# Kernel tuning notes

Hardware: AMD Instinct MI355X
Metric: run time of the kernel (lower is better)

Reference implementation:

```python
import jax, jax.numpy as jnp
import numpy as np
from jax import lax

B, D, N = 1024, 1024, 65536
M, Ks, DS = 8, 256, 128      # key PQ: subvectors, codewords, subvec dim (D/M)
MV, DV = 8, 256              # value PQ: subvectors, subvec dim (OUT/MV)
OUT = MV * DV
K_TOP = 64


def setup_inputs() -> dict:
    key = jax.random.key(0)
    ks = jax.random.split(key, 7)
    x = jax.random.normal(ks[0], (B, D), dtype=jnp.float32)
    # whitening matrix starts as identity in the module; perturb slightly for a non-trivial test
    whitening_matrix = jnp.eye(D, dtype=jnp.float32) + 0.01 * jax.random.normal(ks[1], (D, D), dtype=jnp.float32)
    key_codebooks = jax.random.normal(ks[2], (M, Ks, DS), dtype=jnp.float32)
    value_codebooks = jax.random.normal(ks[3], (MV, Ks, DV), dtype=jnp.float32)
    bias = jnp.zeros((OUT,), dtype=jnp.float32)
    key_codes = jax.random.randint(ks[4], (N, M), 0, Ks, dtype=jnp.int32)
    value_codes = jax.random.randint(ks[5], (N, MV), 0, Ks, dtype=jnp.int32)
    return {
        "x": x,
        "whitening_matrix": whitening_matrix,
        "key_codebooks": key_codebooks,
        "value_codebooks": value_codebooks,
        "bias": bias,
        "key_codes": key_codes,
        "value_codes": value_codes,
        "k": K_TOP,
    }


def reference(x, whitening_matrix, key_codebooks, value_codebooks, bias, key_codes, value_codes, k):
    # 1) whiten the query (module buffer 'whitening_matrix')
    q = x @ whitening_matrix                      # [B, D]
    qs = q.reshape(B, M, DS)                      # [B, M, DS] query subvectors

    # 2) ADC distance tables: squared L2 between each query subvector and each codeword
    #    dt[b, m, c] = ||qs[b,m] - cb[m,c]||^2
    q_sq = jnp.sum(qs * qs, axis=-1)              # [B, M]
    c_sq = jnp.sum(key_codebooks * key_codebooks, axis=-1)  # [M, Ks]
    cross = jnp.einsum("bmd,mcd->bmc", qs, key_codebooks)   # [B, M, Ks]
    dt = q_sq[:, :, None] + c_sq[None, :, :] - 2.0 * cross  # [B, M, Ks]

    # 3) asymmetric distance to all N stored keys via code gather (irregular access)
    lut = dt.transpose(1, 0, 2)                   # [M, B, Ks]
    # per-subvector gather then sum: d[b, n] = sum_m lut[m, b, key_codes[n, m]]
    dists = jax.vmap(lambda l, c: l[:, c])(lut, key_codes.T).sum(axis=0)  # [B, N]

    # 4) top-k nearest neighbors
    neg_top, top_idx = lax.top_k(-dists, k)       # [B, k]

    # 5) reconstruct values of retrieved neighbors from value PQ codebooks
    vc = value_codes[top_idx]                     # [B, k, MV] int codes
    vals = value_codebooks[jnp.arange(MV)[None, None, :], vc]  # [B, k, MV, DV]
    vals = vals.reshape(vals.shape[0], vals.shape[1], OUT)      # [B, k, OUT]

    # 6) distance-weighted aggregation (softmax over negative distances) + bias
    w = jax.nn.softmax(neg_top, axis=-1)          # [B, k]
    y = jnp.einsum("bk,bko->bo", w, vals) + bias  # [B, OUT]
    return y
```

## Files before the change

### kernel.cpp

```cpp
#include <hip/hip_runtime.h>

#define N_ITEMS 65536

__launch_bounds__(256)
__global__ void gemm_q_kernel(const float* __restrict__ A,
                              const float* __restrict__ W,
                              float* __restrict__ qpart) {
  __shared__ float As[16][132];
  __shared__ float Bs[16][132];
  const int tid = threadIdx.x;
  const int tx = tid & 15, ty = tid >> 4;
  const int rb = blockIdx.y * 128, cb = blockIdx.x * 128;
  const int kz = blockIdx.z * 256;
  const int ar = tid >> 2, ac = (tid & 3) << 2;
  const int bk = tid >> 5, bc = (tid & 31) << 2;

  float4 va0 = *(const float4*)&A[(rb + ar) * 1024 + kz + ac];
  float4 va1 = *(const float4*)&A[(rb + ar + 64) * 1024 + kz + ac];
  float4 vb0 = *(const float4*)&W[(kz + bk) * 1024 + cb + bc];
  float4 vb1 = *(const float4*)&W[(kz + bk + 8) * 1024 + cb + bc];

  float acc[8][8] = {};
  for (int k0 = 0; k0 < 256; k0 += 16) {
    As[ac + 0][ar] = va0.x; As[ac + 1][ar] = va0.y;
    As[ac + 2][ar] = va0.z; As[ac + 3][ar] = va0.w;
    As[ac + 0][ar + 64] = va1.x; As[ac + 1][ar + 64] = va1.y;
    As[ac + 2][ar + 64] = va1.z; As[ac + 3][ar + 64] = va1.w;
    *(float4*)&Bs[bk][bc] = vb0;
    *(float4*)&Bs[bk + 8][bc] = vb1;
    __syncthreads();
    if (k0 + 16 < 256) {
      va0 = *(const float4*)&A[(rb + ar) * 1024 + kz + k0 + 16 + ac];
      va1 = *(const float4*)&A[(rb + ar + 64) * 1024 + kz + k0 + 16 + ac];
      vb0 = *(const float4*)&W[(kz + k0 + 16 + bk) * 1024 + cb + bc];
      vb1 = *(const float4*)&W[(kz + k0 + 16 + bk + 8) * 1024 + cb + bc];
    }
#pragma unroll
    for (int kk = 0; kk < 16; kk++) {
      const float4 a0 = *(const float4*)&As[kk][ty << 2];
      const float4 a1 = *(const float4*)&As[kk][64 + (ty << 2)];
      const float4 b0 = *(const float4*)&Bs[kk][tx << 2];
      const float4 b1 = *(const float4*)&Bs[kk][64 + (tx << 2)];
      const float ar8[8] = {a0.x, a0.y, a0.z, a0.w, a1.x, a1.y, a1.z, a1.w};
      const float br8[8] = {b0.x, b0.y, b0.z, b0.w, b1.x, b1.y, b1.z, b1.w};
#pragma unroll
      for (int r = 0; r < 8; r++)
#pragma unroll
        for (int c = 0; c < 8; c++)
          acc[r][c] = fmaf(ar8[r], br8[c], acc[r][c]);
    }
    __syncthreads();
  }
  float* outp = qpart + blockIdx.z * 1048576;
#pragma unroll
  for (int rh = 0; rh < 2; rh++)
#pragma unroll
    for (int r = 0; r < 4; r++) {
      const int row = rb + rh * 64 + (ty << 2) + r;
      const int ri = rh * 4 + r;
      *(float4*)&outp[row * 1024 + cb + (tx << 2)] =
          make_float4(acc[ri][0], acc[ri][1], acc[ri][2], acc[ri][3]);
      *(float4*)&outp[row * 1024 + cb + 64 + (tx << 2)] =
          make_float4(acc[ri][4], acc[ri][5], acc[ri][6], acc[ri][7]);
    }
}

__launch_bounds__(256)
__global__ void lut_kernel(const float* __restrict__ qpart,
                           const float* __restrict__ kcb,
                           const int* __restrict__ key_codes,
                           float* __restrict__ lut,
                           unsigned long long* __restrict__ pcodes,
                           uint4* __restrict__ poffs) {
  if (blockIdx.z == 8) {
    const int g0 = (((int)blockIdx.y * 4 + (int)blockIdx.x) * 256 + (int)threadIdx.x) * 4;
#pragma unroll
    for (int t = 0; t < 4; t++) {
      const int gid = g0 + t;
      unsigned long long p = 0ull;
      unsigned h[8];
#pragma unroll
      for (int j = 0; j < 8; j++) {
        const unsigned c = (unsigned)key_codes[gid * 8 + j] & 255u;
        p |= (unsigned long long)c << (8 * j);
        h[j] = ((c >> 1) << 7) | ((c & 1u) << 2);
      }
      pcodes[gid] = p;
      poffs[gid] = make_uint4(h[0] | (h[1] << 16), h[2] | (h[3] << 16),
                              h[4] | (h[5] << 16), h[6] | (h[7] << 16));
    }
    return;
  }

  __shared__ float As[32][68];
  __shared__ float Bs[32][68];
  const int tid = threadIdx.x;
  const int tx = tid & 15, ty = tid >> 4;
  const int m = blockIdx.z;
  const int rb = blockIdx.y * 64;
  const int cb0 = blockIdx.x * 64;
  float acc[4][4] = {};
  float qa[4] = {}, cs[4] = {};
  for (int k0 = 0; k0 < 128; k0 += 32) {
#pragma unroll
    for (int l = 0; l < 2; l++) {
      const int e = tid + l * 256;
      const int row = e >> 3, c4 = (e & 7) << 2;
      const int qidx = (rb + row) * 1024 + m * 128 + k0 + c4;
      const float4 p0 = *(const float4*)&qpart[qidx];
      const float4 p1 = *(const float4*)&qpart[qidx + 1048576];
      const float4 p2 = *(const float4*)&qpart[qidx + 2097152];
      const float4 p3 = *(const float4*)&qpart[qidx + 3145728];
      const float4 va = make_float4(p0.x + p1.x + p2.x + p3.x,
                                    p0.y + p1.y + p2.y + p3.y,
                                    p0.z + p1.z + p2.z + p3.z,
                                    p0.w + p1.w + p2.w + p3.w);
      As[c4 + 0][row] = va.x; As[c4 + 1][row] = va.y;
      As[c4 + 2][row] = va.z; As[c4 + 3][row] = va.w;
      const float4 vb = *(const float4*)&kcb[(m * 256 + cb0 + row) * 128 + k0 + c4];
      Bs[c4 + 0][row] = vb.x; Bs[c4 + 1][row] = vb.y;
      Bs[c4 + 2][row] = vb.z; Bs[c4 + 3][row] = vb.w;
    }
    __syncthreads();
#pragma unroll
    for (int kk = 0; kk < 32; kk++) {
      const float4 a = *(const float4*)&As[kk][ty << 2];
      const float4 b = *(const float4*)&Bs[kk][tx << 2];
      const float ar[4] = {a.x, a.y, a.z, a.w};
      const float br[4] = {b.x, b.y, b.z, b.w};
#pragma unroll
      for (int r = 0; r < 4; r++)
#pragma unroll
        for (int c = 0; c < 4; c++)
          acc[r][c] = fmaf(ar[r], br[c], acc[r][c]);
#pragma unroll
      for (int r = 0; r < 4; r++) qa[r] = fmaf(ar[r], ar[r], qa[r]);
#pragma unroll
      for (int c = 0; c < 4; c++) cs[c] = fmaf(br[c], br[c], cs[c]);
    }
    __syncthreads();
  }
#pragma unroll
  for (int r = 0; r < 4; r++) {
    const int row = rb + (ty << 2) + r;
    const int col = cb0 + (tx << 2);
    float4 v;
    v.x = qa[r] + cs[0] - 2.0f * acc[r][0];
    v.y = qa[r] + cs[1] - 2.0f * acc[r][1];
    v.z = qa[r] + cs[2] - 2.0f * acc[r][2];
    v.w = qa[r] + cs[3] - 2.0f * acc[r][3];
    *(float4*)&lut[row * 2048 + m * 256 + col] = v;
  }
}

extern __shared__ char dyn_lds[];

__launch_bounds__(1024)
__global__ void scan2r_kernel(const float* __restrict__ lut,
                              const uint4* __restrict__ poffs,
                              unsigned* __restrict__ cand_d,
                              unsigned short* __restrict__ cand_n) {
  char* repb = dyn_lds;
  unsigned* repw = (unsigned*)dyn_lds;
  short* temps = (short*)(dyn_lds + 131072);
  unsigned* tempw = (unsigned*)(dyn_lds + 131072);
  const int tid = threadIdx.x;
  const int g = blockIdx.x;

  {
    const int w = tid >> 6, lane = tid & 63;
    const int rr = w & 1, seg = w >> 1;
    const int row = (g << 1) + rr;
    const int e0 = seg * 256 + lane * 4;
    const float4 v4 = *(const float4*)&lut[row * 2048 + e0];
    float s4 = v4.x + v4.y + v4.z + v4.w;
#pragma unroll
    for (int off = 32; off > 0; off >>= 1) s4 += __shfl_xor(s4, off);
    const float mean = s4 * (1.0f / 256.0f);
    const float vals[4] = {v4.x, v4.y, v4.z, v4.w};
#pragma unroll
    for (int k = 0; k < 4; k++) {
      float f = (vals[k] - mean) * 64.0f;
      f = fmaxf(fminf(f, 32000.0f), -32000.0f);
      temps[(e0 + k) * 2 + rr] = (short)(int)rintf(f);
    }
  }
  __syncthreads();

  {
    const int lane = tid & 63;
    const unsigned v0 = tempw[tid * 2];
    const unsigned v1 = tempw[tid * 2 + 1];
    const int Dbase = tid * 32;
#pragma unroll
    for (int k = 0; k < 16; k++) {
      const int r = (k + lane) & 15;
      repw[Dbase + 2 * r] = v0;
      repw[Dbase + 1 + 2 * r] = v1;
    }
  }
  __syncthreads();

  const int r = tid & 15;
  const char* base0 = repb + (r << 3);
  const char* base1 = repb + 65536 + (r << 3);
  int d0a = 0x7FFFFFFF, d1a = 0x7FFFFFFF, i0a = 0, i1a = 0;
  int d0b = 0x7FFFFFFF, d1b = 0x7FFFFFFF, i0b = 0, i1b = 0;

  uint4 oc = poffs[tid];
  uint4 nc = poffs[tid + 1024];
  for (int it = 0; it < 64; it++) {
    const int n = tid + (it << 10);
    uint4 nn2 = nc;
    if (it < 62) nn2 = poffs[n + 2048];
    unsigned wv;
    int s0, s1;
    wv = *(const unsigned*)(base0 + (oc.x & 0xFFFFu));
    s0 = (int)(short)wv; s1 = ((int)wv) >> 16;
#define LK(B, HV, OFS) { wv = *(const unsigned*)((B) + (HV) + (OFS)); \
    s0 += (int)(short)wv; s1 += ((int)wv) >> 16; }
    LK(base0, oc.x >> 16, 16384)
    LK(base0, oc.y & 0xFFFFu, 32768)
    LK(base0, oc.y >> 16, 49152)
    LK(base1, oc.z & 0xFFFFu, 0)
    LK(base1, oc.z >> 16, 16384)
    LK(base1, oc.w & 0xFFFFu, 32768)
    LK(base1, oc.w >> 16, 49152)
#undef LK
    if (s0 < d1a) {
      if (s0 < d0a) { d1a = d0a; i1a = i0a; d0a = s0; i0a = n; }
      else          { d1a = s0; i1a = n; }
    }
    if (s1 < d1b) {
      if (s1 < d0b) { d1b = d0b; i1b = i0b; d0b = s1; i0b = n; }
      else          { d1b = s1; i1b = n; }
    }
    oc = nc; nc = nn2;
  }

  {
    const int ba = (g << 1) * 2048 + tid * 2;
    *(uint2*)&cand_d[ba] = make_uint2((unsigned)(d0a + 0x40000000),
                                      (unsigned)(d1a + 0x40000000));
    *(unsigned*)&cand_n[ba] = (unsigned)i0a | ((unsigned)i1a << 16);
    const int bb = ((g << 1) + 1) * 2048 + tid * 2;
    *(uint2*)&cand_d[bb] = make_uint2((unsigned)(d0b + 0x40000000),
                                      (unsigned)(d1b + 0x40000000));
    *(unsigned*)&cand_n[bb] = (unsigned)i0b | ((unsigned)i1b << 16);
  }
}

__launch_bounds__(512)
__global__ void scan16_kernel(const float* __restrict__ lut,
                              const unsigned long long* __restrict__ pcodes,
                              unsigned* __restrict__ cand_d,
                              unsigned short* __restrict__ cand_n) {
  __shared__ short sRep[32768];
  const int tid = threadIdx.x;
  const int b = blockIdx.x;

  const float4 v4 = *(const float4*)&lut[b * 2048 + tid * 4];
  float s4 = v4.x + v4.y + v4.z + v4.w;
#pragma unroll
  for (int off = 32; off > 0; off >>= 1) s4 += __shfl_xor(s4, off);
  const float mean = s4 * (1.0f / 256.0f);

  const float vals[4] = {v4.x, v4.y, v4.z, v4.w};
#pragma unroll
  for (int k2 = 0; k2 < 4; k2++) {
    float f = (vals[k2] - mean) * 64.0f;
    f = fmaxf(fminf(f, 32000.0f), -32000.0f);
    const int iv = (int)rintf(f);
    const unsigned hw = (unsigned)(unsigned short)iv;
    const unsigned wrd = hw | (hw << 16);
    const uint4 wv = make_uint4(wrd, wrd, wrd, wrd);
    const int e = tid * 4 + k2;
    *(uint4*)&((unsigned*)sRep)[e * 8] = wv;
    *(uint4*)&((unsigned*)sRep)[e * 8 + 4] = wv;
  }
  __syncthreads();

  const int r = tid & 15;
  int d0 = 0x7FFFFFFF, d1 = 0x7FFFFFFF, d2 = 0x7FFFFFFF, d3 = 0x7FFFFFFF;
  int i0 = 0, i1 = 0, i2 = 0, i3 = 0;

  unsigned long long c8 = pcodes[tid];
  for (int it = 0; it < 128; it++) {
    const int n = tid + (it << 9);
    unsigned long long nxt = 0ull;
    if (it < 127) nxt = pcodes[n + 512];
    const unsigned lo = (unsigned)c8;
    const unsigned hi = (unsigned)(c8 >> 32);
    int s;
    s  = sRep[(((lo      ) & 255u) << 4) + r        ];
    s += sRep[(((lo >>  8) & 255u) << 4) + r +  4096];
    s += sRep[(((lo >> 16) & 255u) << 4) + r +  8192];
    s += sRep[(((lo >> 24)       ) << 4) + r + 12288];
    s += sRep[(((hi      ) & 255u) << 4) + r + 16384];
    s += sRep[(((hi >>  8) & 255u) << 4) + r + 20480];
    s += sRep[(((hi >> 16) & 255u) << 4) + r + 24576];
    s += sRep[(((hi >> 24)       ) << 4) + r + 28672];
    if (s < d3) {
      if (s < d1) {
        if (s < d0) { d3 = d2; i3 = i2; d2 = d1; i2 = i1; d1 = d0; i1 = i0; d0 = s; i0 = n; }
        else        { d3 = d2; i3 = i2; d2 = d1; i2 = i1; d1 = s; i1 = n; }
      } else {
        if (s < d2) { d3 = d2; i3 = i2; d2 = s; i2 = n; }
        else        { d3 = s; i3 = n; }
      }
    }
    c8 = nxt;
  }

  const int base = b * 2048 + tid * 4;
  const uint4 dv = make_uint4((unsigned)(d0 + 0x40000000), (unsigned)(d1 + 0x40000000),
                              (unsigned)(d2 + 0x40000000), (unsigned)(d3 + 0x40000000));
  *(uint4*)&cand_d[base] = dv;
  const unsigned ni01 = (unsigned)i0 | ((unsigned)i1 << 16);
  const unsigned ni23 = (unsigned)i2 | ((unsigned)i3 << 16);
  *(uint2*)&cand_n[base] = make_uint2(ni01, ni23);
}

__launch_bounds__(256)
__global__ void select_kernel(const unsigned* __restrict__ cand_d,
                              const unsigned short* __restrict__ cand_n,
                              const int* __restrict__ value_codes,
                              const float* __restrict__ vcb,
                              const float* __restrict__ bias,
                              float* __restrict__ out) {
  __shared__ unsigned sredw[4];
  __shared__ unsigned long long clist[256];
  __shared__ float sw[256];
  __shared__ int svc[2048];
  __shared__ int scnt;
  __shared__ float sWsum;

  const int tid = threadIdx.x;
  const int b = blockIdx.x;

  const uint4 a0 = *(const uint4*)&cand_d[b * 2048 + tid * 8];
  const uint4 a1 = *(const uint4*)&cand_d[b * 2048 + tid * 8 + 4];
  const uint4 nn = *(const uint4*)&cand_n[b * 2048 + tid * 8];
  unsigned dk[8] = {a0.x, a0.y, a0.z, a0.w, a1.x, a1.y, a1.z, a1.w};
  unsigned ni[8] = {nn.x & 0xFFFFu, nn.x >> 16, nn.y & 0xFFFFu, nn.y >> 16,
                    nn.z & 0xFFFFu, nn.z >> 16, nn.w & 0xFFFFu, nn.w >> 16};

  if (tid == 0) scnt = 0;
  unsigned mn = dk[0];
#pragma unroll
  for (int j = 1; j < 8; j++) mn = (dk[j] < mn) ? dk[j] : mn;
#pragma unroll
  for (int off = 32; off > 0; off >>= 1) {
    const unsigned o = __shfl_xor(mn, off);
    mn = (o < mn) ? o : mn;
  }
  if ((tid & 63) == 0) sredw[tid >> 6] = mn;
  __syncthreads();
  unsigned sMin = sredw[0];
  sMin = (sredw[1] < sMin) ? sredw[1] : sMin;
  sMin = (sredw[2] < sMin) ? sredw[2] : sMin;
  sMin = (sredw[3] < sMin) ? sredw[3] : sMin;
  const unsigned lim = sMin + 2048u;

  const int lane = tid & 63;
  const unsigned long long lm = (1ull << lane) - 1ull;
#pragma unroll
  for (int j = 0; j < 8; j++) {
    const bool pred = dk[j] <= lim;
    const unsigned long long mask = __ballot(pred);
    int base = 0;
    if (lane == 0 && mask) base = atomicAdd(&scnt, __popcll(mask));
    base = __shfl(base, 0);
    if (pred) {
      const int pos = base + __popcll(mask & lm);
      if (pos < 256) clist[pos] = ((unsigned long long)dk[j] << 32) | ni[j];
    }
  }
  __syncthreads();
  const int cnt = min(scnt, 256);

  if (tid < cnt) {
    const int gap = (int)((unsigned)(clist[tid] >> 32)) - (int)sMin;
    sw[tid] = __expf((float)gap * -0.015625f);
  }
  for (int i = tid; i < (cnt << 3); i += 256)
    svc[i] = value_codes[((int)(clist[i >> 3] & 0xFFFFFFFFu)) * 8 + (i & 7)];
  __syncthreads();

  if (tid < 64) {
    float s = 0.f;
    for (int j = tid; j < cnt; j += 64) s += sw[j];
#pragma unroll
    for (int off = 32; off > 0; off >>= 1) s += __shfl_xor(s, off);
    if (tid == 0) sWsum = s;
  }
  __syncthreads();
  const float inv = 1.0f / sWsum;

  const int c0 = tid << 3;
  const int mv = c0 >> 8;
  const int off = c0 & 255;
  float4 acc0 = make_float4(0.f, 0.f, 0.f, 0.f);
  float4 acc1 = make_float4(0.f, 0.f, 0.f, 0.f);
  const float* vbase = vcb + mv * 65536 + off;
  for (int k = 0; k < cnt; k++) {
    const float w = sw[k];
    const float* vp = vbase + svc[(k << 3) + mv] * 256;
    const float4 v0 = *(const float4*)vp;
    const float4 v1 = *(const float4*)(vp + 4);
    acc0.x = fmaf(w, v0.x, acc0.x); acc0.y = fmaf(w, v0.y, acc0.y);
    acc0.z = fmaf(w, v0.z, acc0.z); acc0.w = fmaf(w, v0.w, acc0.w);
    acc1.x = fmaf(w, v1.x, acc1.x); acc1.y = fmaf(w, v1.y, acc1.y);
    acc1.z = fmaf(w, v1.z, acc1.z); acc1.w = fmaf(w, v1.w, acc1.w);
  }
  const float4 b0 = *(const float4*)&bias[c0];
  const float4 b1 = *(const float4*)&bias[c0 + 4];
  *(float4*)&out[b * 2048 + c0] =
      make_float4(fmaf(acc0.x, inv, b0.x), fmaf(acc0.y, inv, b0.y),
                  fmaf(acc0.z, inv, b0.z), fmaf(acc0.w, inv, b0.w));
  *(float4*)&out[b * 2048 + c0 + 4] =
      make_float4(fmaf(acc1.x, inv, b1.x), fmaf(acc1.y, inv, b1.y),
                  fmaf(acc1.z, inv, b1.z), fmaf(acc1.w, inv, b1.w));
}

extern "C" void kernel_launch(void* const* d_in, const int* in_sizes, int n_in,
                              void* d_out, int out_size, void* d_ws, size_t ws_size,
                              hipStream_t stream) {
  const float* x    = (const float*)d_in[0];
  const float* W    = (const float*)d_in[1];
  const float* kcb  = (const float*)d_in[2];
  const float* vcb  = (const float*)d_in[3];
  const float* bias = (const float*)d_in[4];
  const int* key_codes   = (const int*)d_in[5];
  const int* value_codes = (const int*)d_in[6];
  float* out = (float*)d_out;

  float* qpart = (float*)d_ws;
  float* lut   = qpart + 4194304;
  uint4* poffs = (uint4*)(lut + 2097152);
  unsigned long long* pcodes = (unsigned long long*)(poffs + 65536);
  unsigned* cand_d = (unsigned*)d_ws;
  unsigned short* cand_n = (unsigned short*)(cand_d + 2097152);

  hipLaunchKernelGGL(gemm_q_kernel, dim3(8, 8, 4), dim3(256), 0, stream,
                     x, W, qpart);
  hipLaunchKernelGGL(lut_kernel, dim3(4, 16, 9), dim3(256), 0, stream,
                     qpart, kcb, key_codes, lut, pcodes, poffs);

  const hipError_t attr_rc = hipFuncSetAttribute(
      (const void*)scan2r_kernel, hipFuncAttributeMaxDynamicSharedMemorySize, 139264);
  if (attr_rc == hipSuccess) {
    hipLaunchKernelGGL(scan2r_kernel, dim3(512), dim3(1024), 139264, stream,
                       lut, poffs, cand_d, cand_n);
  } else {
    hipLaunchKernelGGL(scan16_kernel, dim3(1024), dim3(512), 0, stream,
                       lut, pcodes, cand_d, cand_n);
  }

  hipLaunchKernelGGL(select_kernel, dim3(1024), dim3(256), 0, stream,
                     cand_d, cand_n, value_codes, vcb, bias, out);
}
```

Before: 196.2 us.

## Scan four query rows per block with 64-bit LDS lookups and packed top-2 keys

The scan kernel now handles four query rows per block instead of two. Each LDS lookup becomes a 64-bit load that returns four int16 partial distances, so the number of table reads per row is halved. Top-2 tracking is rewritten as branchless min/max over packed keys that combine distance and iteration index, replacing the data-dependent branches. The cost is half as many blocks (256), a larger shared-memory footprint per block, and the packed key truncating distances to about 26 bits.

```diff
diff --git a/kernel.cpp b/kernel.cpp
--- a/kernel.cpp
+++ b/kernel.cpp
@@ -83,7 +83,7 @@
       for (int j = 0; j < 8; j++) {
         const unsigned c = (unsigned)key_codes[gid * 8 + j] & 255u;
         p |= (unsigned long long)c << (8 * j);
-        h[j] = ((c >> 1) << 7) | ((c & 1u) << 2);
+        h[j] = ((c >> 1) << 7) | ((c & 1u) << 3);
       }
       pcodes[gid] = p;
       poffs[gid] = make_uint4(h[0] | (h[1] << 16), h[2] | (h[3] << 16),
@@ -156,97 +156,110 @@
 extern __shared__ char dyn_lds[];
 
 __launch_bounds__(1024)
-__global__ void scan2r_kernel(const float* __restrict__ lut,
+__global__ void scan4r_kernel(const float* __restrict__ lut,
                               const uint4* __restrict__ poffs,
                               unsigned* __restrict__ cand_d,
                               unsigned short* __restrict__ cand_n) {
   char* repb = dyn_lds;
-  unsigned* repw = (unsigned*)dyn_lds;
   short* temps = (short*)(dyn_lds + 131072);
-  unsigned* tempw = (unsigned*)(dyn_lds + 131072);
+  unsigned long long* tempq = (unsigned long long*)(dyn_lds + 131072);
   const int tid = threadIdx.x;
   const int g = blockIdx.x;
 
   {
     const int w = tid >> 6, lane = tid & 63;
-    const int rr = w & 1, seg = w >> 1;
-    const int row = (g << 1) + rr;
-    const int e0 = seg * 256 + lane * 4;
-    const float4 v4 = *(const float4*)&lut[row * 2048 + e0];
-    float s4 = v4.x + v4.y + v4.z + v4.w;
-#pragma unroll
-    for (int off = 32; off > 0; off >>= 1) s4 += __shfl_xor(s4, off);
-    const float mean = s4 * (1.0f / 256.0f);
-    const float vals[4] = {v4.x, v4.y, v4.z, v4.w};
-#pragma unroll
-    for (int k = 0; k < 4; k++) {
-      float f = (vals[k] - mean) * 64.0f;
-      f = fmaxf(fminf(f, 32000.0f), -32000.0f);
-      temps[(e0 + k) * 2 + rr] = (short)(int)rintf(f);
+#pragma unroll
+    for (int t0 = 0; t0 < 2; t0++) {
+      const int t = w + t0 * 16;
+      const int rr = t & 3, seg = t >> 2;
+      const int row = (g << 2) + rr;
+      const int e0 = seg * 256 + lane * 4;
+      const float4 v4 = *(const float4*)&lut[row * 2048 + e0];
+      float s4 = v4.x + v4.y + v4.z + v4.w;
+#pragma unroll
+      for (int off = 32; off > 0; off >>= 1) s4 += __shfl_xor(s4, off);
+      const float mean = s4 * (1.0f / 256.0f);
+      const float vals[4] = {v4.x, v4.y, v4.z, v4.w};
+#pragma unroll
+      for (int k = 0; k < 4; k++) {
+        float f = (vals[k] - mean) * 64.0f;
+        f = fmaxf(fminf(f, 32000.0f), -32000.0f);
+        temps[(e0 + k) * 4 + rr] = (short)(int)rintf(f);
+      }
     }
   }
   __syncthreads();
 
   {
     const int lane = tid & 63;
-    const unsigned v0 = tempw[tid * 2];
-    const unsigned v1 = tempw[tid * 2 + 1];
-    const int Dbase = tid * 32;
-#pragma unroll
-    for (int k = 0; k < 16; k++) {
-      const int r = (k + lane) & 15;
-      repw[Dbase + 2 * r] = v0;
-      repw[Dbase + 1 + 2 * r] = v1;
-    }
-  }
-  __syncthreads();
-
-  const int r = tid & 15;
-  const char* base0 = repb + (r << 3);
-  const char* base1 = repb + 65536 + (r << 3);
-  int d0a = 0x7FFFFFFF, d1a = 0x7FFFFFFF, i0a = 0, i1a = 0;
-  int d0b = 0x7FFFFFFF, d1b = 0x7FFFFFFF, i0b = 0, i1b = 0;
+    const unsigned long long q0 = tempq[tid * 2];
+    const unsigned long long q1 = tempq[tid * 2 + 1];
+    const uint4 wv = make_uint4((unsigned)q0, (unsigned)(q0 >> 32),
+                                (unsigned)q1, (unsigned)(q1 >> 32));
+    uint4* repv = (uint4*)dyn_lds;
+    const int base = tid * 8;
+#pragma unroll
+    for (int k = 0; k < 8; k++) {
+      const int r = (k + lane) & 7;
+      repv[base + r] = wv;
+    }
+  }
+  __syncthreads();
+
+  const int r = tid & 7;
+  const char* base0 = repb + (r << 4);
+  const char* base1 = repb + 65536 + (r << 4);
+  unsigned k0[4], k1[4];
+#pragma unroll
+  for (int j = 0; j < 4; j++) { k0[j] = 0xFFFFFFFFu; k1[j] = 0xFFFFFFFFu; }
 
   uint4 oc = poffs[tid];
   uint4 nc = poffs[tid + 1024];
   for (int it = 0; it < 64; it++) {
-    const int n = tid + (it << 10);
     uint4 nn2 = nc;
-    if (it < 62) nn2 = poffs[n + 2048];
-    unsigned wv;
-    int s0, s1;
-    wv = *(const unsigned*)(base0 + (oc.x & 0xFFFFu));
-    s0 = (int)(short)wv; s1 = ((int)wv) >> 16;
-#define LK(B, HV, OFS) { wv = *(const unsigned*)((B) + (HV) + (OFS)); \
-    s0 += (int)(short)wv; s1 += ((int)wv) >> 16; }
-    LK(base0, oc.x >> 16, 16384)
-    LK(base0, oc.y & 0xFFFFu, 32768)
-    LK(base0, oc.y >> 16, 49152)
-    LK(base1, oc.z & 0xFFFFu, 0)
-    LK(base1, oc.z >> 16, 16384)
-    LK(base1, oc.w & 0xFFFFu, 32768)
-    LK(base1, oc.w >> 16, 49152)
-#undef LK
-    if (s0 < d1a) {
-      if (s0 < d0a) { d1a = d0a; i1a = i0a; d0a = s0; i0a = n; }
-      else          { d1a = s0; i1a = n; }
-    }
-    if (s1 < d1b) {
-      if (s1 < d0b) { d1b = d0b; i1b = i0b; d0b = s1; i0b = n; }
-      else          { d1b = s1; i1b = n; }
+    if (it < 62) nn2 = poffs[tid + (it << 10) + 2048];
+    int s0, s1, s2, s3;
+    {
+      const unsigned long long wv = *(const unsigned long long*)(base0 + (oc.x & 0xFFFFu));
+      const unsigned lo = (unsigned)wv, hi = (unsigned)(wv >> 32);
+      s0 = (int)(short)lo; s1 = ((int)lo) >> 16;
+      s2 = (int)(short)hi; s3 = ((int)hi) >> 16;
+    }
+#define LK4(B, HV, OFS) { \
+    const unsigned long long wv = *(const unsigned long long*)((B) + (HV) + (OFS)); \
+    const unsigned lo = (unsigned)wv, hi = (unsigned)(wv >> 32);                    \
+    s0 += (int)(short)lo; s1 += ((int)lo) >> 16;                                    \
+    s2 += (int)(short)hi; s3 += ((int)hi) >> 16; }
+    LK4(base0, oc.x >> 16, 16384)
+    LK4(base0, oc.y & 0xFFFFu, 32768)
+    LK4(base0, oc.y >> 16, 49152)
+    LK4(base1, oc.z & 0xFFFFu, 0)
+    LK4(base1, oc.z >> 16, 16384)
+    LK4(base1, oc.w & 0xFFFFu, 32768)
+    LK4(base1, oc.w >> 16, 49152)
+#undef LK4
+    const int ss[4] = {s0, s1, s2, s3};
+#pragma unroll
+    for (int j = 0; j < 4; j++) {
+      const unsigned key = ((unsigned)(ss[j] + 0x40000) << 6) | (unsigned)it;
+      const unsigned mx = (k0[j] > key) ? k0[j] : key;
+      k0[j] = (k0[j] < key) ? k0[j] : key;
+      k1[j] = (k1[j] < mx) ? k1[j] : mx;
     }
     oc = nc; nc = nn2;
   }
 
-  {
-    const int ba = (g << 1) * 2048 + tid * 2;
-    *(uint2*)&cand_d[ba] = make_uint2((unsigned)(d0a + 0x40000000),
-                                      (unsigned)(d1a + 0x40000000));
-    *(unsigned*)&cand_n[ba] = (unsigned)i0a | ((unsigned)i1a << 16);
-    const int bb = ((g << 1) + 1) * 2048 + tid * 2;
-    *(uint2*)&cand_d[bb] = make_uint2((unsigned)(d0b + 0x40000000),
-                                      (unsigned)(d1b + 0x40000000));
-    *(unsigned*)&cand_n[bb] = (unsigned)i0b | ((unsigned)i1b << 16);
+#pragma unroll
+  for (int j = 0; j < 4; j++) {
+    const int row = (g << 2) + j;
+    const int d0 = (int)(k0[j] >> 6) - 0x40000;
+    const int d1 = (int)(k1[j] >> 6) - 0x40000;
+    const int n0 = tid + (int)((k0[j] & 63u) << 10);
+    const int n1 = tid + (int)((k1[j] & 63u) << 10);
+    const int ba = row * 2048 + tid * 2;
+    *(uint2*)&cand_d[ba] = make_uint2((unsigned)(d0 + 0x40000000),
+                                      (unsigned)(d1 + 0x40000000));
+    *(unsigned*)&cand_n[ba] = (unsigned)n0 | ((unsigned)n1 << 16);
   }
 }
 
@@ -448,9 +461,9 @@
                      qpart, kcb, key_codes, lut, pcodes, poffs);
 
   const hipError_t attr_rc = hipFuncSetAttribute(
-      (const void*)scan2r_kernel, hipFuncAttributeMaxDynamicSharedMemorySize, 139264);
+      (const void*)scan4r_kernel, hipFuncAttributeMaxDynamicSharedMemorySize, 147456);
   if (attr_rc == hipSuccess) {
-    hipLaunchKernelGGL(scan2r_kernel, dim3(512), dim3(1024), 139264, stream,
+    hipLaunchKernelGGL(scan4r_kernel, dim3(256), dim3(1024), 147456, stream,
                        lut, poffs, cand_d, cand_n);
   } else {
     hipLaunchKernelGGL(scan16_kernel, dim3(1024), dim3(512), 0, stream,
```

Result: faster. 187.4 us (-4.5%).
